# Performance work log

Hardware: AMD Instinct MI355X
Metric: run time of the kernel (lower is better)

The kernel has to match this reference:

```python
import jax, jax.numpy as jnp
import numpy as np

TWO_PI = 2.0 * np.pi

def ringify(x):
    # wrap values to [-pi, pi)
    return (x + np.pi) % TWO_PI - np.pi

def complex_mean(x, axes):
    # circular mean direction: atan2(sum sin, sum ringify(cos))
    dir_x = ringify(jnp.cos(x)).sum(axis=axes)
    dir_y = jnp.sin(x).sum(axis=axes)
    return jnp.arctan2(dir_y, dir_x)

def setup_inputs() -> dict:
    key = jax.random.key(0)
    k1, k2, k3, k4 = jax.random.split(key, 4)
    B = 4096
    return {
        "x": jax.random.normal(k1, (B, 1, 28, 28), dtype=jnp.float32),
        "conv1_w": jax.random.normal(k2, (4, 1, 2, 2), dtype=jnp.float32),
        "conv2_w": jax.random.normal(k3, (8, 4, 4, 4), dtype=jnp.float32),
        "ff_w": jax.random.normal(k4, (288, 10), dtype=jnp.float32),
    }

def reference(x, conv1_w, conv2_w, ff_w):
    B = x.shape[0]
    x = ringify(x).reshape(B, 1, 28, 28)

    # --- ring conv1: 2x2 kernel, stride 2 (non-overlapping patches) ---
    # [B,1,28,28] -> [B,14,14,1,2,2]  (matches unfold(2,2,2).unfold(3,2,2).permute)
    p1 = x.reshape(B, 1, 14, 2, 14, 2).transpose(0, 2, 4, 1, 3, 5)
    w1 = conv1_w.transpose(1, 2, 3, 0)            # [1,2,2,4]
    d1 = ringify(p1[..., None] - w1)              # [B,14,14,1,2,2,4]
    h1 = complex_mean(d1, (3, 4, 5))              # [B,14,14,4]

    # --- ring conv2: 4x4 kernel, stride 2 (overlapping patches) ---
    h1 = h1.transpose(0, 3, 1, 2)                 # [B,4,14,14]
    idx = (jnp.arange(6) * 2)[:, None] + jnp.arange(4)[None, :]  # [6,4] window rows/cols
    p2 = h1[:, :, idx, :][:, :, :, :, idx]        # [B,4,6,4,6,4]
    p2 = p2.transpose(0, 2, 4, 1, 3, 5)           # [B,6,6,4,4,4]
    w2 = conv2_w.transpose(1, 2, 3, 0)            # [4,4,4,8]
    d2 = ringify(p2[..., None] - w2)              # [B,6,6,4,4,4,8]
    h2 = complex_mean(d2, (3, 4, 5))              # [B,6,6,8]

    # --- ring feed-forward ---
    f = h2.reshape(B, 288)
    d3 = ringify(f[:, :, None] - ff_w)            # [B,288,10]
    out = complex_mean(d3, (1,))                  # [B,10]
    return jnp.sin(out)
```

## Files before the change

### kernel.cpp

```cpp
#include <hip/hip_runtime.h>
#include <math.h>

#define FFT_OFF 0
#define W2_OFF 2880
#define W1_OFF 3400

__global__ void precompute_trig(const float* __restrict__ w1,
                                const float* __restrict__ w2,
                                const float* __restrict__ ff,
                                float2* __restrict__ ws) {
    int idx = blockIdx.x * blockDim.x + threadIdx.x;
    if (idx < 2880) {
        int k = idx / 10, n = idx % 10;
        float s, c; sincosf(ff[idx], &s, &c);
        ws[FFT_OFF + n * 288 + k] = make_float2(c, s);
    } else if (idx < 3392) {
        int i = idx - 2880;
        int oc = i >> 6, e = i & 63;
        float s, c; sincosf(w2[i], &s, &c);
        ws[W2_OFF + (oc >> 1) * 130 + e * 2 + (oc & 1)] = make_float2(c, s);
    } else if (idx < 3408) {
        int i = idx - 3392;
        float s, c; sincosf(w1[i], &s, &c);
        ws[W1_OFF + i] = make_float2(c, s);
    }
}

__device__ __forceinline__ void conv1_pos(float2 r0, float2 r1,
                                          const float2* __restrict__ w1t,
                                          float2* __restrict__ sc1,
                                          int pi, int pj) {
    float sx[4], cx[4];
    __sincosf(r0.x, &sx[0], &cx[0]);
    __sincosf(r0.y, &sx[1], &cx[1]);
    __sincosf(r1.x, &sx[2], &cx[2]);
    __sincosf(r1.y, &sx[3], &cx[3]);
    #pragma unroll
    for (int oc = 0; oc < 4; oc++) {
        float4 wa = *(const float4*)(w1t + oc * 4);
        float4 wb = *(const float4*)(w1t + oc * 4 + 2);
        float Y = 0.f, X = 0.f;
        Y = fmaf(sx[0], wa.x, fmaf(-cx[0], wa.y, Y));
        X = fmaf(cx[0], wa.x, fmaf( sx[0], wa.y, X));
        Y = fmaf(sx[1], wa.z, fmaf(-cx[1], wa.w, Y));
        X = fmaf(cx[1], wa.z, fmaf( sx[1], wa.w, X));
        Y = fmaf(sx[2], wb.x, fmaf(-cx[2], wb.y, Y));
        X = fmaf(cx[2], wb.x, fmaf( sx[2], wb.y, X));
        Y = fmaf(sx[3], wb.z, fmaf(-cx[3], wb.w, Y));
        X = fmaf(cx[3], wb.z, fmaf( sx[3], wb.w, X));
        float inv = rsqrtf(fmaxf(fmaf(X, X, Y * Y), 1e-30f));
        sc1[oc * 252 + pi * 18 + pj] = make_float2(Y * inv, X * inv);
    }
}

__global__ __launch_bounds__(128, 4) void ringnn_kernel(
    const float* __restrict__ x,
    const float2* __restrict__ ws,
    float* __restrict__ out)
{
    __shared__ __align__(16) float2 trig2[520];
    __shared__ __align__(16) float2 sc1[1008];
    __shared__ __align__(16) float2 sc2[288];
    const int tid = threadIdx.x;
    const float2* __restrict__ fft = ws + FFT_OFF;
    const float2* __restrict__ w1t = ws + W1_OFF;

    const float* xb = x + (size_t)blockIdx.x * 784;
    const int pi0 = tid / 14, pj0 = tid % 14;
    float2 a0 = *(const float2*)(xb + (2 * pi0) * 28 + 2 * pj0);
    float2 a1 = *(const float2*)(xb + (2 * pi0 + 1) * 28 + 2 * pj0);
    const int p1 = tid + 128;
    int pi1 = 0, pj1 = 0;
    float2 b0 = make_float2(0.f, 0.f), b1 = make_float2(0.f, 0.f);
    if (p1 < 196) {
        pi1 = p1 / 14; pj1 = p1 % 14;
        b0 = *(const float2*)(xb + (2 * pi1) * 28 + 2 * pj1);
        b1 = *(const float2*)(xb + (2 * pi1 + 1) * 28 + 2 * pj1);
    }

    for (int i = tid; i < 260; i += 128)
        ((float4*)trig2)[i] = ((const float4*)(ws + W2_OFF))[i];

    conv1_pos(a0, a1, w1t, sc1, pi0, pj0);
    if (p1 < 196) conv1_pos(b0, b1, w1t, sc1, pi1, pj1);
    __syncthreads();

    if (tid < 96) {
        int r = tid;
        int oi = r >> 4, ojg = (r >> 3) & 1, ocp = (r >> 1) & 3, hf = r & 1;
        const float2* wbp = trig2 + ocp * 130;
        float aY[3][2] = {{0.f,0.f},{0.f,0.f},{0.f,0.f}};
        float aX[3][2] = {{0.f,0.f},{0.f,0.f},{0.f,0.f}};
        #pragma unroll
        for (int ch = 0; ch < 4; ch++) {
            #pragma unroll
            for (int kk = 0; kk < 2; kk++) {
                int ki = hf * 2 + kk;
                int base = ch * 252 + (oi * 2 + ki) * 18 + ojg * 6;
                float4 f0 = *(const float4*)(sc1 + base);
                float4 f1 = *(const float4*)(sc1 + base + 2);
                float4 f2 = *(const float4*)(sc1 + base + 4);
                float4 f3 = *(const float4*)(sc1 + base + 6);
                float ss[8] = {f0.x,f0.z,f1.x,f1.z,f2.x,f2.z,f3.x,f3.z};
                float cc[8] = {f0.y,f0.w,f1.y,f1.w,f2.y,f2.w,f3.y,f3.w};
                int e0 = ch * 16 + ki * 4;
                #pragma unroll
                for (int kj = 0; kj < 4; kj++) {
                    float4 wv = *(const float4*)(wbp + (e0 + kj) * 2);
                    #pragma unroll
                    for (int ojl = 0; ojl < 3; ojl++) {
                        float s = ss[ojl * 2 + kj], c = cc[ojl * 2 + kj];
                        aY[ojl][0] = fmaf(s, wv.x, fmaf(-c, wv.y, aY[ojl][0]));
                        aX[ojl][0] = fmaf(c, wv.x, fmaf( s, wv.y, aX[ojl][0]));
                        aY[ojl][1] = fmaf(s, wv.z, fmaf(-c, wv.w, aY[ojl][1]));
                        aX[ojl][1] = fmaf(c, wv.z, fmaf( s, wv.w, aX[ojl][1]));
                    }
                }
            }
        }
        #pragma unroll
        for (int ojl = 0; ojl < 3; ojl++) {
            float y0 = aY[ojl][0]; y0 += __shfl_xor(y0, 1);
            float y1 = aY[ojl][1]; y1 += __shfl_xor(y1, 1);
            float x0 = aX[ojl][0]; x0 += __shfl_xor(x0, 1);
            float x1 = aX[ojl][1]; x1 += __shfl_xor(x1, 1);
            float Y = hf ? y1 : y0;
            float X = hf ? x1 : x0;
            float inv = rsqrtf(fmaxf(fmaf(X, X, Y * Y), 1e-30f));
            int p = oi * 6 + ojg * 3 + ojl;
            sc2[p * 8 + ocp * 2 + hf] = make_float2(Y * inv, X * inv);
        }
    }
    __syncthreads();

    #pragma unroll
    for (int rr = 0; rr < 3; rr++) {
        int idx = tid + (rr << 7);
        if (idx < 320) {
            int n = idx >> 5, s = idx & 31;
            const float2* wn = fft + n * 288;
            float Y = 0.f, X = 0.f;
            #pragma unroll
            for (int i = 0; i < 9; i++) {
                int k = i * 32 + s;
                float2 sc = sc2[k];
                float2 w = wn[k];
                Y = fmaf(sc.x, w.x, fmaf(-sc.y, w.y, Y));
                X = fmaf(sc.y, w.x, fmaf( sc.x, w.y, X));
            }
            #pragma unroll
            for (int off = 16; off > 0; off >>= 1) {
                Y += __shfl_down(Y, off, 32);
                X += __shfl_down(X, off, 32);
            }
            if (s == 0) {
                out[(size_t)blockIdx.x * 10 + n] =
                    Y * rsqrtf(fmaxf(fmaf(X, X, Y * Y), 1e-30f));
            }
        }
    }
}

extern "C" void kernel_launch(void* const* d_in, const int* in_sizes, int n_in,
                              void* d_out, int out_size, void* d_ws, size_t ws_size,
                              hipStream_t stream) {
    const float* x  = (const float*)d_in[0];
    const float* w1 = (const float*)d_in[1];
    const float* w2 = (const float*)d_in[2];
    const float* ff = (const float*)d_in[3];
    float* out = (float*)d_out;
    const int B = in_sizes[0] / 784;

    float2* ws = (float2*)d_ws;
    precompute_trig<<<14, 256, 0, stream>>>(w1, w2, ff, ws);
    ringnn_kernel<<<B, 128, 0, stream>>>(x, ws, out);
}
```

Measured before the change: 85.01 us.

## Process two images per block with 256 threads

Each block now handles two images with 256 threads instead of one image with 128, doubling the shared-memory buffers and remapping the threads of every stage across both images. This is meant to raise thread utilization (392 conv1 positions over 256 threads, 192 active threads in conv2) and to share the conv2 weight-table load between two images. In exchange each block uses more shared memory, and odd batch sizes would drop the last image.

Measured after the change: 82.39 us. 1.03x faster.

```diff
diff --git a/kernel.cpp b/kernel.cpp
--- a/kernel.cpp
+++ b/kernel.cpp
@@ -53,42 +53,48 @@
     }
 }
 
-__global__ __launch_bounds__(128, 4) void ringnn_kernel(
+__global__ __launch_bounds__(256, 4) void ringnn_kernel(
     const float* __restrict__ x,
     const float2* __restrict__ ws,
     float* __restrict__ out)
 {
     __shared__ __align__(16) float2 trig2[520];
-    __shared__ __align__(16) float2 sc1[1008];
-    __shared__ __align__(16) float2 sc2[288];
+    __shared__ __align__(16) float2 sc1[2 * 1008];
+    __shared__ __align__(16) float2 sc2[2 * 288];
     const int tid = threadIdx.x;
     const float2* __restrict__ fft = ws + FFT_OFF;
     const float2* __restrict__ w1t = ws + W1_OFF;
+    const size_t img0 = (size_t)blockIdx.x * 2;
 
-    const float* xb = x + (size_t)blockIdx.x * 784;
-    const int pi0 = tid / 14, pj0 = tid % 14;
-    float2 a0 = *(const float2*)(xb + (2 * pi0) * 28 + 2 * pj0);
-    float2 a1 = *(const float2*)(xb + (2 * pi0 + 1) * 28 + 2 * pj0);
-    const int p1 = tid + 128;
+    const int im0 = (tid >= 196) ? 1 : 0;
+    const int p0  = tid - im0 * 196;
+    const int pi0 = p0 / 14, pj0 = p0 % 14;
+    const float* xb0 = x + (img0 + im0) * 784;
+    float2 a0 = *(const float2*)(xb0 + (2 * pi0) * 28 + 2 * pj0);
+    float2 a1 = *(const float2*)(xb0 + (2 * pi0 + 1) * 28 + 2 * pj0);
     int pi1 = 0, pj1 = 0;
     float2 b0 = make_float2(0.f, 0.f), b1 = make_float2(0.f, 0.f);
-    if (p1 < 196) {
-        pi1 = p1 / 14; pj1 = p1 % 14;
-        b0 = *(const float2*)(xb + (2 * pi1) * 28 + 2 * pj1);
-        b1 = *(const float2*)(xb + (2 * pi1 + 1) * 28 + 2 * pj1);
+    if (tid < 136) {
+        int p = tid + 60;
+        pi1 = p / 14; pj1 = p % 14;
+        const float* xb1 = x + (img0 + 1) * 784;
+        b0 = *(const float2*)(xb1 + (2 * pi1) * 28 + 2 * pj1);
+        b1 = *(const float2*)(xb1 + (2 * pi1 + 1) * 28 + 2 * pj1);
     }
 
-    for (int i = tid; i < 260; i += 128)
+    for (int i = tid; i < 260; i += 256)
         ((float4*)trig2)[i] = ((const float4*)(ws + W2_OFF))[i];
 
-    conv1_pos(a0, a1, w1t, sc1, pi0, pj0);
-    if (p1 < 196) conv1_pos(b0, b1, w1t, sc1, pi1, pj1);
+    conv1_pos(a0, a1, w1t, sc1 + im0 * 1008, pi0, pj0);
+    if (tid < 136) conv1_pos(b0, b1, w1t, sc1 + 1008, pi1, pj1);
     __syncthreads();
 
-    if (tid < 96) {
-        int r = tid;
+    if (tid < 192) {
+        const int img = (tid >= 96) ? 1 : 0;
+        int r = tid - img * 96;
         int oi = r >> 4, ojg = (r >> 3) & 1, ocp = (r >> 1) & 3, hf = r & 1;
         const float2* wbp = trig2 + ocp * 130;
+        const float2* s1p = sc1 + img * 1008;
         float aY[3][2] = {{0.f,0.f},{0.f,0.f},{0.f,0.f}};
         float aX[3][2] = {{0.f,0.f},{0.f,0.f},{0.f,0.f}};
         #pragma unroll
@@ -97,10 +103,10 @@
             for (int kk = 0; kk < 2; kk++) {
                 int ki = hf * 2 + kk;
                 int base = ch * 252 + (oi * 2 + ki) * 18 + ojg * 6;
-                float4 f0 = *(const float4*)(sc1 + base);
-                float4 f1 = *(const float4*)(sc1 + base + 2);
-                float4 f2 = *(const float4*)(sc1 + base + 4);
-                float4 f3 = *(const float4*)(sc1 + base + 6);
+                float4 f0 = *(const float4*)(s1p + base);
+                float4 f1 = *(const float4*)(s1p + base + 2);
+                float4 f2 = *(const float4*)(s1p + base + 4);
+                float4 f3 = *(const float4*)(s1p + base + 6);
                 float ss[8] = {f0.x,f0.z,f1.x,f1.z,f2.x,f2.z,f3.x,f3.z};
                 float cc[8] = {f0.y,f0.w,f1.y,f1.w,f2.y,f2.w,f3.y,f3.w};
                 int e0 = ch * 16 + ki * 4;
@@ -128,22 +134,25 @@
             float X = hf ? x1 : x0;
             float inv = rsqrtf(fmaxf(fmaf(X, X, Y * Y), 1e-30f));
             int p = oi * 6 + ojg * 3 + ojl;
-            sc2[p * 8 + ocp * 2 + hf] = make_float2(Y * inv, X * inv);
+            sc2[img * 288 + p * 8 + ocp * 2 + hf] = make_float2(Y * inv, X * inv);
         }
     }
     __syncthreads();
 
     #pragma unroll
     for (int rr = 0; rr < 3; rr++) {
-        int idx = tid + (rr << 7);
-        if (idx < 320) {
+        int t = tid + (rr << 8);
+        if (t < 640) {
+            int img = (t >= 320) ? 1 : 0;
+            int idx = t - img * 320;
             int n = idx >> 5, s = idx & 31;
             const float2* wn = fft + n * 288;
+            const float2* s2p = sc2 + img * 288;
             float Y = 0.f, X = 0.f;
             #pragma unroll
             for (int i = 0; i < 9; i++) {
                 int k = i * 32 + s;
-                float2 sc = sc2[k];
+                float2 sc = s2p[k];
                 float2 w = wn[k];
                 Y = fmaf(sc.x, w.x, fmaf(-sc.y, w.y, Y));
                 X = fmaf(sc.y, w.x, fmaf( sc.x, w.y, X));
@@ -154,7 +163,7 @@
                 X += __shfl_down(X, off, 32);
             }
             if (s == 0) {
-                out[(size_t)blockIdx.x * 10 + n] =
+                out[(img0 + img) * 10 + n] =
                     Y * rsqrtf(fmaxf(fmaf(X, X, Y * Y), 1e-30f));
             }
         }
@@ -173,5 +182,5 @@
 
     float2* ws = (float2*)d_ws;
     precompute_trig<<<14, 256, 0, stream>>>(w1, w2, ff, ws);
-    ringnn_kernel<<<B, 128, 0, stream>>>(x, ws, out);
+    ringnn_kernel<<<B / 2, 256, 0, stream>>>(x, ws, out);
 }
```
